# Performance work log

Measured on AMD Instinct MI355X. Metric: run time of the kernel, lower is better.

The kernel has to match this reference:

```python
import jax, jax.numpy as jnp
import numpy as np

H = 12          # num_heads
E = 768         # key_dim
LORA_SCALE = 32.0 / 4.0  # scale / R
NEG = -1e9


def setup_inputs() -> dict:
    key = jax.random.key(0)
    ks = jax.random.split(key, 8)
    B, L = 2, 2048
    return {
        "x": jax.random.normal(ks[0], (B, L, E), jnp.float32),
        "w_in": jax.random.normal(ks[1], (E, 3 * E), jnp.float32) * 0.02,
        "b_in": jnp.zeros((3 * E,), jnp.float32),
        "A_in": jax.random.normal(ks[2], (4, 3 * E), jnp.float32) * 0.02,
        "B_in": jax.random.normal(ks[3], (E, 4), jnp.float32) * 0.02,
        "w_out": jax.random.normal(ks[4], (E, E), jnp.float32) * 0.02,
        "b_out": jnp.zeros((E,), jnp.float32),
        "A_out": jax.random.normal(ks[5], (4, E), jnp.float32) * 0.02,
        "B_out": jax.random.normal(ks[6], (E, 4), jnp.float32) * 0.02,
    }


def reference(x, w_in, b_in, A_in, B_in, w_out, b_out, A_out, B_out):
    Bb, L, _ = x.shape
    D = E // H
    # LoRA-adapted input projection: w + (scale/R) * B @ A
    w1 = w_in + LORA_SCALE * (B_in @ A_in)          # [E, 3E]
    c = jnp.einsum('ble,eo->blo', x, w1) + b_in      # [B, L, 3E]
    q, k, v = jnp.split(c, 3, axis=2)
    # split heads -> [B, H, L, D]
    def heads(t):
        return t.reshape(Bb, L, H, D).transpose(0, 2, 1, 3)
    q, k, v = heads(q), heads(k), heads(v)
    # attention scores (no 1/sqrt(d): scale=False in module defaults)
    w = jnp.einsum('bhqd,bhkd->bhqk', q, k)          # [B, H, L, L]
    band = jnp.tril(jnp.ones((L, L), jnp.float32))   # causal band
    w = w * band + NEG * (1.0 - band)
    w = jax.nn.softmax(w, axis=-1)
    a = jnp.einsum('bhqk,bhkd->bhqd', w, v)          # [B, H, L, D]
    a = a.transpose(0, 2, 1, 3).reshape(Bb, L, E)    # merge heads
    w2 = w_out + LORA_SCALE * (B_out @ A_out)        # [E, E]
    return jnp.einsum('ble,eo->blo', a, w2) + b_out
```

## Files before the change

### kernel.cpp

```cpp
#include <hip/hip_runtime.h>
#include <hip/hip_bf16.h>

#define BB 2
#define LL 2048
#define EE 768
#define HH 12
#define DD 64
#define N3 2304
#define TOK 4096
#define LOG2E 1.4426950408889634f

typedef __attribute__((ext_vector_type(8))) short short8;
typedef __attribute__((ext_vector_type(4))) short s16x4;
typedef __attribute__((ext_vector_type(4))) float f32x4;
typedef __attribute__((ext_vector_type(4))) unsigned int uix4;
typedef unsigned int uint_t;
typedef unsigned short ushort_t;

__device__ __forceinline__ f32x4 mfma16(short8 a, short8 b, f32x4 c) {
  return __builtin_amdgcn_mfma_f32_16x16x32_bf16(a, b, c, 0, 0, 0);
}
__device__ __forceinline__ f32x4 mfma16k16(s16x4 a, s16x4 b, f32x4 c) {
  return __builtin_amdgcn_mfma_f32_16x16x16bf16_1k(a, b, c, 0, 0, 0);
}

__device__ __forceinline__ ushort_t bf16bits(float f) {
  __hip_bfloat16 h = __float2bfloat16(f);
  return *reinterpret_cast<ushort_t*>(&h);
}

__device__ __forceinline__ uint_t pack2bf(float a, float b) {
  return (uint_t)bf16bits(a) | ((uint_t)bf16bits(b) << 16);
}

__device__ __forceinline__ float bits2f(ushort_t u) {
  union { uint_t u; float f; } cv;
  cv.u = ((uint_t)u) << 16;
  return cv.f;
}

__device__ __forceinline__ void stage64(const __hip_bfloat16* gbase, int ldg,
                                        short* lds, int tid) {
  const int wave = tid >> 6, lane = tid & 63;
#pragma unroll
  for (int c = 0; c < 4; ++c) {
    int off = c * 4096 + wave * 1024 + lane * 16;
    int row = off >> 7;
    int cs  = (off & 127) >> 4;
    int cc  = cs ^ (row & 7);
    __builtin_amdgcn_global_load_lds(
        (const __attribute__((address_space(1))) void*)((const short*)gbase + (size_t)row * ldg + cc * 8),
        (__attribute__((address_space(3))) void*)(lds + c * 2048 + wave * 512),
        16, 0, 0);
  }
}

__device__ __forceinline__ void stage128(const __hip_bfloat16* gbase, int ldg,
                                         short* lds, int tid) {
  const int wave = tid >> 6, lane = tid & 63;
#pragma unroll
  for (int c = 0; c < 4; ++c) {
    int off = c * 4096 + wave * 1024 + lane * 16;
    int row = off >> 8;
    int cs  = (off & 255) >> 4;
    int cc  = cs ^ (row & 7);
    __builtin_amdgcn_global_load_lds(
        (const __attribute__((address_space(1))) void*)((const short*)gbase + (size_t)row * ldg + cc * 8),
        (__attribute__((address_space(3))) void*)(lds + c * 2048 + wave * 512),
        16, 0, 0);
  }
}

__device__ __forceinline__ short8 frag64(const short* lds, int row, int chunk) {
  return *(const short8*)(lds + row * 64 + (chunk ^ (row & 7)) * 8);
}

__global__ void prep_kernel(const float* __restrict__ x, const float* __restrict__ w_in,
                            const float* __restrict__ A_in, const float* __restrict__ B_in,
                            const float* __restrict__ w_out, const float* __restrict__ A_out,
                            const float* __restrict__ B_out,
                            __hip_bfloat16* __restrict__ xb, __hip_bfloat16* __restrict__ w1T,
                            __hip_bfloat16* __restrict__ w2T) {
  __shared__ float tile[32][33];
  const int bid = blockIdx.x, t = threadIdx.x;
  if (bid < 2304) {
    const float *W, *Am, *Bm;
    __hip_bfloat16* out;
    int N, tx, ty;
    if (bid < 1728) { W = w_in;  Am = A_in;  Bm = B_in;  out = w1T; N = N3; tx = bid % 72; ty = bid / 72; }
    else { int jj = bid - 1728; W = w_out; Am = A_out; Bm = B_out; out = w2T; N = EE; tx = jj % 24; ty = jj / 24; }
    const int e0 = ty * 32, o0 = tx * 32;
    const int r = t >> 5, col = t & 31;
#pragma unroll
    for (int i = 0; i < 4; ++i)
      tile[r + i * 8][col] = W[(size_t)(e0 + r + i * 8) * N + (o0 + col)];
    __syncthreads();
    const int e = e0 + col;
    const float b0 = Bm[e * 4 + 0], b1 = Bm[e * 4 + 1], b2 = Bm[e * 4 + 2], b3 = Bm[e * 4 + 3];
#pragma unroll
    for (int i = 0; i < 4; ++i) {
      const int o = o0 + r + i * 8;
      float acc = b0 * Am[o] + b1 * Am[N + o] + b2 * Am[2 * N + o] + b3 * Am[3 * N + o];
      out[(size_t)o * EE + e] = __float2bfloat16(tile[col][r + i * 8] + 8.0f * acc);
    }
  } else {
    const int j = bid - 2304;
    const float* src = x + (size_t)j * 4096 + t * 16;
    short* dst = (short*)xb + (size_t)j * 4096 + t * 16;
#pragma unroll
    for (int half = 0; half < 2; ++half) {
      float4 a = ((const float4*)src)[half * 2];
      float4 b = ((const float4*)src)[half * 2 + 1];
      short8 v;
      v[0] = (short)bf16bits(a.x); v[1] = (short)bf16bits(a.y);
      v[2] = (short)bf16bits(a.z); v[3] = (short)bf16bits(a.w);
      v[4] = (short)bf16bits(b.x); v[5] = (short)bf16bits(b.y);
      v[6] = (short)bf16bits(b.z); v[7] = (short)bf16bits(b.w);
      ((short8*)dst)[half] = v;
    }
  }
}

template<bool F32OUT, bool QSCALE, bool SPLITV>
__global__ __launch_bounds__(256, 2) void gemm_bt(const __hip_bfloat16* __restrict__ A,
                                                  const __hip_bfloat16* __restrict__ BT,
                                                  const float* __restrict__ bias,
                                                  void* __restrict__ outp,
                                                  __hip_bfloat16* __restrict__ vTp,
                                                  int M, int N, int K) {
  __shared__ __align__(16) short Al[128 * 64];
  __shared__ __align__(16) short Bl[128 * 64];
  const int tid = threadIdx.x, lane = tid & 63, wave = tid >> 6;
  const int quad = lane >> 4, c16 = lane & 15;
  const int n0 = blockIdx.x * 128, m0 = blockIdx.y * 128;
  const int msub = (wave & 1) * 64, nsub = (wave >> 1) * 64;
  f32x4 acc[4][4] = {};
  for (int k0 = 0; k0 < K; k0 += 64) {
    __syncthreads();
    stage64(A + (size_t)m0 * K + k0, K, Al, tid);
    stage64(BT + (size_t)n0 * K + k0, K, Bl, tid);
    __syncthreads();
#pragma unroll
    for (int ks = 0; ks < 2; ++ks) {
      short8 af[4], bfr[4];
#pragma unroll
      for (int i = 0; i < 4; ++i) {
        af[i]  = frag64(Al, msub + i * 16 + c16, ks * 4 + quad);
        bfr[i] = frag64(Bl, nsub + i * 16 + c16, ks * 4 + quad);
      }
#pragma unroll
      for (int mi = 0; mi < 4; ++mi)
#pragma unroll
        for (int ni = 0; ni < 4; ++ni)
          acc[mi][ni] = mfma16(af[mi], bfr[ni], acc[mi][ni]);
    }
  }
  if (SPLITV && n0 >= 2 * EE) {
    const int bofs = (m0 >> 11) * EE;
    const int l0 = (m0 & 2047) + msub;
#pragma unroll
    for (int ni = 0; ni < 4; ++ni) {
      int n = n0 + nsub + ni * 16 + c16;
      float bv = bias[n];
      const size_t rowbase = (size_t)(bofs + (n - 2 * EE)) * LL;
#pragma unroll
      for (int mi = 0; mi < 4; ++mi) {
        int l = l0 + mi * 16 + quad * 4;
        uint2 w;
        w.x = pack2bf(acc[mi][ni][0] + bv, acc[mi][ni][1] + bv);
        w.y = pack2bf(acc[mi][ni][2] + bv, acc[mi][ni][3] + bv);
        *(uint2*)((short*)vTp + rowbase + l) = w;
      }
    }
    return;
  }
#pragma unroll
  for (int ni = 0; ni < 4; ++ni) {
    int n = n0 + nsub + ni * 16 + c16;
    float bv = bias[n];
    float sc = (QSCALE && n < EE) ? LOG2E : 1.0f;
#pragma unroll
    for (int mi = 0; mi < 4; ++mi) {
      int row0 = m0 + msub + mi * 16 + quad * 4;
#pragma unroll
      for (int r = 0; r < 4; ++r) {
        float v = (acc[mi][ni][r] + bv) * sc;
        if (F32OUT) ((float*)outp)[(size_t)(row0 + r) * N + n] = v;
        else ((__hip_bfloat16*)outp)[(size_t)(row0 + r) * N + n] = __float2bfloat16(v);
      }
    }
  }
}

#define SLOT_BYTES 16896
union pk4 { uint_t u[2]; s16x4 s4; };

__global__ __launch_bounds__(256, 2) void attn_kernel(const __hip_bfloat16* __restrict__ qkv,
                                                      const __hip_bfloat16* __restrict__ vT,
                                                      char* __restrict__ Opart,
                                                      __hip_bfloat16* __restrict__ abuf) {
  __shared__ __align__(16) short Kl[2 * 128 * 64];
  __shared__ __align__(16) short Vl[2 * 64 * 128];
  const int tid = threadIdx.x, lane = tid & 63, wave = tid >> 6;
  const int quad = lane >> 4, c16 = lane & 15;
  const int bid = blockIdx.x;
  const int bh = bid % 24;
  const int j = bid / 24;
  int qt, cch;
  if (j < 8)       { qt = 8 + j;  cch = 0; }
  else if (j < 16) { qt = 23 - j; cch = 1; }
  else             { qt = 23 - j; cch = 0; }
  const int b = bh / HH, h = bh % HH;
  const int q0 = qt * 128;
  const int qw = q0 + wave * 32;
  const int ks = cch * 1024;
  const int ke = min(q0 + 128, ks + 1024);
  const int niter = (ke - ks + 127) >> 7;
  short8 qfA[2], qfB[2];
  {
    const short* qra = (const short*)qkv + (size_t)(b * LL + qw + c16) * N3 + h * DD;
    qfA[0] = *(const short8*)(qra + quad * 8);
    qfA[1] = *(const short8*)(qra + 32 + quad * 8);
    const short* qrb = qra + 16 * N3;
    qfB[0] = *(const short8*)(qrb + quad * 8);
    qfB[1] = *(const short8*)(qrb + 32 + quad * 8);
  }
  float lA = 0.f, lB = 0.f;
  f32x4 oA[4] = {}, oB[4] = {};
  const int vsub = (quad & 1) * 4;
  const int cxor = (c16 & 7);
  const __hip_bfloat16* kgbase = qkv + (size_t)(b * LL) * N3 + EE + h * DD;
  const __hip_bfloat16* vgbase = vT + (size_t)((b * HH + h) * DD) * LL;
  stage64(kgbase + (size_t)ks * N3, N3, Kl, tid);
  stage128(vgbase + ks, LL, Vl, tid);
  for (int it = 0; it < niter; ++it) {
    const int k0 = ks + it * 128;
    __syncthreads();
    if (it + 1 < niter) {
      short* Kn = Kl + ((it + 1) & 1) * 8192;
      short* Vn = Vl + ((it + 1) & 1) * 8192;
      stage64(kgbase + (size_t)(k0 + 128) * N3, N3, Kn, tid);
      stage128(vgbase + k0 + 128, LL, Vn, tid);
    }
    const short* Kb = Kl + (it & 1) * 8192;
    const short* Vb = Vl + (it & 1) * 8192;
    int nlimB = (qw + 31 - k0) / 16 + 1; if (nlimB > 8) nlimB = 8;
    int nlimA = (qw + 15 - k0) / 16 + 1; if (nlimA > 8) nlimA = 8;
#pragma unroll
    for (int nt = 0; nt < 8; ++nt) {
      if (nt < nlimB) {
        const short* krow = Kb + (nt * 16 + c16) * 64;
        const int kc0 = (quad ^ cxor) * 8;
        short8 kf0 = *(const short8*)(krow + kc0);
        short8 kf1 = *(const short8*)(krow + (kc0 ^ 32));
        const int kb = k0 + nt * 16 + quad * 4;
        const bool diag = (k0 + nt * 16 + 15 > qw + 16);
        f32x4 sB = {};
        sB = mfma16(kf0, qfB[0], sB);
        sB = mfma16(kf1, qfB[1], sB);
        if (diag) {
          const int q = qw + 16 + c16;
#pragma unroll
          for (int r = 0; r < 4; ++r)
            if (kb + r > q) sB[r] = -1e9f;
        }
        pk4 pB;
        {
          float p0 = exp2f(sB[0]), p1 = exp2f(sB[1]);
          float p2 = exp2f(sB[2]), p3 = exp2f(sB[3]);
          lB += (p0 + p1) + (p2 + p3);
          pB.u[0] = pack2bf(p0, p1);
          pB.u[1] = pack2bf(p2, p3);
        }
        const bool doA = (nt < nlimA);
        pk4 pA;
        if (doA) {
          f32x4 sA = {};
          sA = mfma16(kf0, qfA[0], sA);
          sA = mfma16(kf1, qfA[1], sA);
          if (k0 + nt * 16 + 15 > qw) {
            const int q = qw + c16;
#pragma unroll
            for (int r = 0; r < 4; ++r)
              if (kb + r > q) sA[r] = -1e9f;
          }
          float p0 = exp2f(sA[0]), p1 = exp2f(sA[1]);
          float p2 = exp2f(sA[2]), p3 = exp2f(sA[3]);
          lA += (p0 + p1) + (p2 + p3);
          pA.u[0] = pack2bf(p0, p1);
          pA.u[1] = pack2bf(p2, p3);
        }
        const int cg = nt * 2 + (quad >> 1);
        const short* vbase = Vb + c16 * 128 + ((cg ^ cxor) * 8 + vsub);
#pragma unroll
        for (int dt = 0; dt < 4; ++dt) {
          s16x4 vf = *(const s16x4*)(vbase + dt * 2048);
          oB[dt] = mfma16k16(vf, pB.s4, oB[dt]);
          if (doA) oA[dt] = mfma16k16(vf, pA.s4, oA[dt]);
        }
      }
    }
  }
  lA += __shfl_xor(lA, 16); lA += __shfl_xor(lA, 32);
  lB += __shfl_xor(lB, 16); lB += __shfl_xor(lB, 32);
  const bool single = (cch == 0) && (qt < 8);
  const float nA = single ? 1.0f / lA : 1.0f;
  const float nB = single ? 1.0f / lB : 1.0f;
  char* op = Opart + (size_t)((bh * 16 + qt) * 2 + cch) * SLOT_BYTES;
  __syncthreads();
  if (!single && quad == 0) {
    float* lout = (float*)(op + 16384);
    lout[wave * 32 + c16] = lA;
    lout[wave * 32 + 16 + c16] = lB;
  }
  short* reg = Kl + wave * 1152;
#pragma unroll
  for (int hh = 0; hh < 2; ++hh) {
    const float sc = hh ? nB : nA;
#pragma unroll
    for (int dt = 0; dt < 4; ++dt) {
      f32x4 o = hh ? oB[dt] : oA[dt];
      uint_t* p = (uint_t*)(reg + c16 * 72 + dt * 16 + quad * 4);
      p[0] = pack2bf(o[0] * sc, o[1] * sc);
      p[1] = pack2bf(o[2] * sc, o[3] * sc);
    }
#pragma unroll
    for (int it = 0; it < 2; ++it) {
      int idx = it * 64 + lane;
      int tq = idx >> 3, c = idx & 7;
      short8 v = *(const short8*)(reg + tq * 72 + c * 8);
      if (single)
        *(short8*)((short*)abuf + (size_t)(b * LL + q0 + wave * 32 + hh * 16 + tq) * EE + h * DD + c * 8) = v;
      else
        *(short8*)((short*)op + (wave * 32 + hh * 16 + tq) * 64 + c * 8) = v;
    }
  }
}

__global__ void merge_kernel(const char* __restrict__ Opart,
                             __hip_bfloat16* __restrict__ abuf) {
  const int t = threadIdx.x;
  const int bh = blockIdx.x >> 3, qt = 8 + (blockIdx.x & 7);
  const int b = bh / HH, h = bh % HH;
  const char* p0 = Opart + (size_t)((bh * 16 + qt) * 2) * SLOT_BYTES;
  const char* p1 = p0 + SLOT_BYTES;
  const int q = t >> 1, dc = (t & 1) * 32;
  float l = ((const float*)(p0 + 16384))[q] + ((const float*)(p1 + 16384))[q];
  const float inv = 1.0f / l;
  const short* o0 = (const short*)p0 + q * 64 + dc;
  const short* o1 = (const short*)p1 + q * 64 + dc;
  __align__(16) short out[32];
#pragma unroll
  for (int blk = 0; blk < 4; ++blk) {
    short8 r0 = *(const short8*)(o0 + blk * 8);
    short8 r1 = *(const short8*)(o1 + blk * 8);
#pragma unroll
    for (int i = 0; i < 8; ++i) {
      float v = bits2f((ushort_t)r0[i]) + bits2f((ushort_t)r1[i]);
      out[blk * 8 + i] = (short)bf16bits(v * inv);
    }
  }
  short* dst = (short*)abuf + (size_t)(b * LL + qt * 128 + q) * EE + h * DD + dc;
#pragma unroll
  for (int blk = 0; blk < 4; ++blk)
    *(short8*)(dst + blk * 8) = *(short8*)(out + blk * 8);
}

extern "C" void kernel_launch(void* const* d_in, const int* in_sizes, int n_in,
                              void* d_out, int out_size, void* d_ws, size_t ws_size,
                              hipStream_t stream) {
  (void)in_sizes; (void)n_in; (void)out_size; (void)ws_size;
  const float* x     = (const float*)d_in[0];
  const float* w_in  = (const float*)d_in[1];
  const float* b_in  = (const float*)d_in[2];
  const float* A_in  = (const float*)d_in[3];
  const float* B_in  = (const float*)d_in[4];
  const float* w_out = (const float*)d_in[5];
  const float* b_out = (const float*)d_in[6];
  const float* A_out = (const float*)d_in[7];
  const float* B_out = (const float*)d_in[8];
  char* ws = (char*)d_ws;
  __hip_bfloat16* xb   = (__hip_bfloat16*)(ws);
  __hip_bfloat16* w1T  = (__hip_bfloat16*)(ws + 6291456);
  __hip_bfloat16* w2T  = (__hip_bfloat16*)(ws + 9830400);
  __hip_bfloat16* qkv  = (__hip_bfloat16*)(ws + 11010048);
  __hip_bfloat16* vT   = (__hip_bfloat16*)(ws + 29884416);
  __hip_bfloat16* abuf = (__hip_bfloat16*)(ws + 36175872);
  char* Opart          = ws + 42467328;

  prep_kernel<<<3072, 256, 0, stream>>>(x, w_in, A_in, B_in, w_out, A_out, B_out,
                                        xb, w1T, w2T);
  gemm_bt<false, true, true><<<dim3(N3 / 128, TOK / 128), 256, 0, stream>>>(
      xb, w1T, b_in, qkv, vT, TOK, N3, EE);
  attn_kernel<<<24 * 24, 256, 0, stream>>>(qkv, vT, Opart, abuf);
  merge_kernel<<<24 * 8, 256, 0, stream>>>(Opart, abuf);
  gemm_bt<true, false, false><<<dim3(EE / 128, TOK / 128), 256, 0, stream>>>(
      abuf, w2T, b_out, d_out, nullptr, TOK, EE, EE);
}
```

Before: 169.6 us.

## Split attention KV into 512-chunks, read K/V directly from global, fast exp2

Attention now splits the key range into up to four 512-token chunks instead of two 1024-token chunks, launching 40 work items per head through lookup tables, with the merge kernel summing up to four partials. The LDS double-buffered staging of K and V is removed: fragments are loaded straight from global memory, which frees shared memory so occupancy can rise (launch bounds 4). exp2f is replaced by the raw v_exp_f32 instruction, and bf16 packing uses a simple bias-add rounding. The aim is better load balance and occupancy, at the cost of uncoalesced, cache-dependent global fragment loads, extra partial-merge traffic, and slightly different rounding (no NaN handling).

Result: slower. 207.3 us (+22.2%).

```diff
diff --git a/kernel.cpp b/kernel.cpp
--- a/kernel.cpp
+++ b/kernel.cpp
@@ -29,8 +29,16 @@
   return *reinterpret_cast<ushort_t*>(&h);
 }
 
-__device__ __forceinline__ uint_t pack2bf(float a, float b) {
-  return (uint_t)bf16bits(a) | ((uint_t)bf16bits(b) << 16);
+__device__ __forceinline__ float fast_exp2(float x) {
+  float r;
+  asm("v_exp_f32 %0, %1" : "=v"(r) : "v"(x));
+  return r;
+}
+
+__device__ __forceinline__ uint_t pack2bf_rn(float a, float b) {
+  uint_t ua = __float_as_uint(a) + 0x8000u;
+  uint_t ub = __float_as_uint(b) + 0x8000u;
+  return (ua >> 16) | (ub & 0xFFFF0000u);
 }
 
 __device__ __forceinline__ float bits2f(ushort_t u) {
@@ -47,22 +55,6 @@
     int off = c * 4096 + wave * 1024 + lane * 16;
     int row = off >> 7;
     int cs  = (off & 127) >> 4;
-    int cc  = cs ^ (row & 7);
-    __builtin_amdgcn_global_load_lds(
-        (const __attribute__((address_space(1))) void*)((const short*)gbase + (size_t)row * ldg + cc * 8),
-        (__attribute__((address_space(3))) void*)(lds + c * 2048 + wave * 512),
-        16, 0, 0);
-  }
-}
-
-__device__ __forceinline__ void stage128(const __hip_bfloat16* gbase, int ldg,
-                                         short* lds, int tid) {
-  const int wave = tid >> 6, lane = tid & 63;
-#pragma unroll
-  for (int c = 0; c < 4; ++c) {
-    int off = c * 4096 + wave * 1024 + lane * 16;
-    int row = off >> 8;
-    int cs  = (off & 255) >> 4;
     int cc  = cs ^ (row & 7);
     __builtin_amdgcn_global_load_lds(
         (const __attribute__((address_space(1))) void*)((const short*)gbase + (size_t)row * ldg + cc * 8),
@@ -167,8 +159,8 @@
       for (int mi = 0; mi < 4; ++mi) {
         int l = l0 + mi * 16 + quad * 4;
         uint2 w;
-        w.x = pack2bf(acc[mi][ni][0] + bv, acc[mi][ni][1] + bv);
-        w.y = pack2bf(acc[mi][ni][2] + bv, acc[mi][ni][3] + bv);
+        w.x = pack2bf_rn(acc[mi][ni][0] + bv, acc[mi][ni][1] + bv);
+        w.y = pack2bf_rn(acc[mi][ni][2] + bv, acc[mi][ni][3] + bv);
         *(uint2*)((short*)vTp + rowbase + l) = w;
       }
     }
@@ -195,26 +187,29 @@
 #define SLOT_BYTES 16896
 union pk4 { uint_t u[2]; s16x4 s4; };
 
-__global__ __launch_bounds__(256, 2) void attn_kernel(const __hip_bfloat16* __restrict__ qkv,
+__device__ const signed char QTAB[40] = {
+  3,4,5,6,7,8,9,10,11,12,13,14,15,  7,8,9,10,11,12,13,14,15,
+  11,12,13,14,15, 15,  2,6,10,14,  1,5,9,13,  0,4,8,12};
+__device__ const signed char CTAB[40] = {
+  0,0,0,0,0,0,0,0,0,0,0,0,0,  1,1,1,1,1,1,1,1,1,
+  2,2,2,2,2, 3,  0,1,2,3,  0,1,2,3,  0,1,2,3};
+
+__global__ __launch_bounds__(256, 4) void attn_kernel(const __hip_bfloat16* __restrict__ qkv,
                                                       const __hip_bfloat16* __restrict__ vT,
                                                       char* __restrict__ Opart,
                                                       __hip_bfloat16* __restrict__ abuf) {
-  __shared__ __align__(16) short Kl[2 * 128 * 64];
-  __shared__ __align__(16) short Vl[2 * 64 * 128];
+  __shared__ __align__(16) short Ep[4 * 1152];
   const int tid = threadIdx.x, lane = tid & 63, wave = tid >> 6;
   const int quad = lane >> 4, c16 = lane & 15;
   const int bid = blockIdx.x;
   const int bh = bid % 24;
   const int j = bid / 24;
-  int qt, cch;
-  if (j < 8)       { qt = 8 + j;  cch = 0; }
-  else if (j < 16) { qt = 23 - j; cch = 1; }
-  else             { qt = 23 - j; cch = 0; }
+  const int qt = QTAB[j], cch = CTAB[j];
   const int b = bh / HH, h = bh % HH;
   const int q0 = qt * 128;
   const int qw = q0 + wave * 32;
-  const int ks = cch * 1024;
-  const int ke = min(q0 + 128, ks + 1024);
+  const int ks = cch * 512;
+  const int ke = min(q0 + 128, ks + 512);
   const int niter = (ke - ks + 127) >> 7;
   short8 qfA[2], qfB[2];
   {
@@ -227,32 +222,18 @@
   }
   float lA = 0.f, lB = 0.f;
   f32x4 oA[4] = {}, oB[4] = {};
-  const int vsub = (quad & 1) * 4;
-  const int cxor = (c16 & 7);
-  const __hip_bfloat16* kgbase = qkv + (size_t)(b * LL) * N3 + EE + h * DD;
-  const __hip_bfloat16* vgbase = vT + (size_t)((b * HH + h) * DD) * LL;
-  stage64(kgbase + (size_t)ks * N3, N3, Kl, tid);
-  stage128(vgbase + ks, LL, Vl, tid);
+  const short* kg = (const short*)qkv + (size_t)(b * LL + c16) * N3 + EE + h * DD + quad * 8;
+  const short* vg = (const short*)vT + (size_t)((b * HH + h) * DD + c16) * LL + quad * 4;
   for (int it = 0; it < niter; ++it) {
     const int k0 = ks + it * 128;
-    __syncthreads();
-    if (it + 1 < niter) {
-      short* Kn = Kl + ((it + 1) & 1) * 8192;
-      short* Vn = Vl + ((it + 1) & 1) * 8192;
-      stage64(kgbase + (size_t)(k0 + 128) * N3, N3, Kn, tid);
-      stage128(vgbase + k0 + 128, LL, Vn, tid);
-    }
-    const short* Kb = Kl + (it & 1) * 8192;
-    const short* Vb = Vl + (it & 1) * 8192;
     int nlimB = (qw + 31 - k0) / 16 + 1; if (nlimB > 8) nlimB = 8;
     int nlimA = (qw + 15 - k0) / 16 + 1; if (nlimA > 8) nlimA = 8;
 #pragma unroll
     for (int nt = 0; nt < 8; ++nt) {
       if (nt < nlimB) {
-        const short* krow = Kb + (nt * 16 + c16) * 64;
-        const int kc0 = (quad ^ cxor) * 8;
-        short8 kf0 = *(const short8*)(krow + kc0);
-        short8 kf1 = *(const short8*)(krow + (kc0 ^ 32));
+        const short* kr = kg + (size_t)(k0 + nt * 16) * N3;
+        short8 kf0 = *(const short8*)(kr);
+        short8 kf1 = *(const short8*)(kr + 32);
         const int kb = k0 + nt * 16 + quad * 4;
         const bool diag = (k0 + nt * 16 + 15 > qw + 16);
         f32x4 sB = {};
@@ -266,11 +247,11 @@
         }
         pk4 pB;
         {
-          float p0 = exp2f(sB[0]), p1 = exp2f(sB[1]);
-          float p2 = exp2f(sB[2]), p3 = exp2f(sB[3]);
+          float p0 = fast_exp2(sB[0]), p1 = fast_exp2(sB[1]);
+          float p2 = fast_exp2(sB[2]), p3 = fast_exp2(sB[3]);
           lB += (p0 + p1) + (p2 + p3);
-          pB.u[0] = pack2bf(p0, p1);
-          pB.u[1] = pack2bf(p2, p3);
+          pB.u[0] = pack2bf_rn(p0, p1);
+          pB.u[1] = pack2bf_rn(p2, p3);
         }
         const bool doA = (nt < nlimA);
         pk4 pA;
@@ -284,17 +265,16 @@
             for (int r = 0; r < 4; ++r)
               if (kb + r > q) sA[r] = -1e9f;
           }
-          float p0 = exp2f(sA[0]), p1 = exp2f(sA[1]);
-          float p2 = exp2f(sA[2]), p3 = exp2f(sA[3]);
+          float p0 = fast_exp2(sA[0]), p1 = fast_exp2(sA[1]);
+          float p2 = fast_exp2(sA[2]), p3 = fast_exp2(sA[3]);
           lA += (p0 + p1) + (p2 + p3);
-          pA.u[0] = pack2bf(p0, p1);
-          pA.u[1] = pack2bf(p2, p3);
+          pA.u[0] = pack2bf_rn(p0, p1);
+          pA.u[1] = pack2bf_rn(p2, p3);
         }
-        const int cg = nt * 2 + (quad >> 1);
-        const short* vbase = Vb + c16 * 128 + ((cg ^ cxor) * 8 + vsub);
+        const short* vb = vg + k0 + nt * 16;
 #pragma unroll
         for (int dt = 0; dt < 4; ++dt) {
-          s16x4 vf = *(const s16x4*)(vbase + dt * 2048);
+          s16x4 vf = *(const s16x4*)(vb + (size_t)dt * 16 * LL);
           oB[dt] = mfma16k16(vf, pB.s4, oB[dt]);
           if (doA) oA[dt] = mfma16k16(vf, pA.s4, oA[dt]);
         }
@@ -303,17 +283,16 @@
   }
   lA += __shfl_xor(lA, 16); lA += __shfl_xor(lA, 32);
   lB += __shfl_xor(lB, 16); lB += __shfl_xor(lB, 32);
-  const bool single = (cch == 0) && (qt < 8);
+  const bool single = (cch == 0) && (qt < 4);
   const float nA = single ? 1.0f / lA : 1.0f;
   const float nB = single ? 1.0f / lB : 1.0f;
-  char* op = Opart + (size_t)((bh * 16 + qt) * 2 + cch) * SLOT_BYTES;
-  __syncthreads();
+  char* op = Opart + (size_t)((bh * 16 + qt) * 4 + cch) * SLOT_BYTES;
   if (!single && quad == 0) {
     float* lout = (float*)(op + 16384);
     lout[wave * 32 + c16] = lA;
     lout[wave * 32 + 16 + c16] = lB;
   }
-  short* reg = Kl + wave * 1152;
+  short* reg = Ep + wave * 1152;
 #pragma unroll
   for (int hh = 0; hh < 2; ++hh) {
     const float sc = hh ? nB : nA;
@@ -321,8 +300,8 @@
     for (int dt = 0; dt < 4; ++dt) {
       f32x4 o = hh ? oB[dt] : oA[dt];
       uint_t* p = (uint_t*)(reg + c16 * 72 + dt * 16 + quad * 4);
-      p[0] = pack2bf(o[0] * sc, o[1] * sc);
-      p[1] = pack2bf(o[2] * sc, o[3] * sc);
+      p[0] = pack2bf_rn(o[0] * sc, o[1] * sc);
+      p[1] = pack2bf_rn(o[2] * sc, o[3] * sc);
     }
 #pragma unroll
     for (int it = 0; it < 2; ++it) {
@@ -340,26 +319,34 @@
 __global__ void merge_kernel(const char* __restrict__ Opart,
                              __hip_bfloat16* __restrict__ abuf) {
   const int t = threadIdx.x;
-  const int bh = blockIdx.x >> 3, qt = 8 + (blockIdx.x & 7);
+  const int bh = blockIdx.x / 12, qt = 4 + (blockIdx.x % 12);
+  const int nch = (qt >> 2) + 1;
   const int b = bh / HH, h = bh % HH;
-  const char* p0 = Opart + (size_t)((bh * 16 + qt) * 2) * SLOT_BYTES;
-  const char* p1 = p0 + SLOT_BYTES;
+  const char* pb = Opart + (size_t)((bh * 16 + qt) * 4) * SLOT_BYTES;
   const int q = t >> 1, dc = (t & 1) * 32;
-  float l = ((const float*)(p0 + 16384))[q] + ((const float*)(p1 + 16384))[q];
+  float l = 0.f;
+  float acc[32];
+#pragma unroll
+  for (int i = 0; i < 32; ++i) acc[i] = 0.f;
+#pragma unroll
+  for (int c = 0; c < 4; ++c) {
+    if (c < nch) {
+      const char* p = pb + (size_t)c * SLOT_BYTES;
+      l += ((const float*)(p + 16384))[q];
+      const short* o = (const short*)p + q * 64 + dc;
+#pragma unroll
+      for (int blk = 0; blk < 4; ++blk) {
+        short8 r = *(const short8*)(o + blk * 8);
+#pragma unroll
+        for (int i = 0; i < 8; ++i) acc[blk * 8 + i] += bits2f((ushort_t)r[i]);
+      }
+    }
+  }
   const float inv = 1.0f / l;
-  const short* o0 = (const short*)p0 + q * 64 + dc;
-  const short* o1 = (const short*)p1 + q * 64 + dc;
   __align__(16) short out[32];
 #pragma unroll
-  for (int blk = 0; blk < 4; ++blk) {
-    short8 r0 = *(const short8*)(o0 + blk * 8);
-    short8 r1 = *(const short8*)(o1 + blk * 8);
-#pragma unroll
-    for (int i = 0; i < 8; ++i) {
-      float v = bits2f((ushort_t)r0[i]) + bits2f((ushort_t)r1[i]);
-      out[blk * 8 + i] = (short)bf16bits(v * inv);
-    }
-  }
+  for (int i = 0; i < 16; ++i)
+    ((uint_t*)out)[i] = pack2bf_rn(acc[2 * i] * inv, acc[2 * i + 1] * inv);
   short* dst = (short*)abuf + (size_t)(b * LL + qt * 128 + q) * EE + h * DD + dc;
 #pragma unroll
   for (int blk = 0; blk < 4; ++blk)
@@ -392,8 +379,8 @@
                                         xb, w1T, w2T);
   gemm_bt<false, true, true><<<dim3(N3 / 128, TOK / 128), 256, 0, stream>>>(
       xb, w1T, b_in, qkv, vT, TOK, N3, EE);
-  attn_kernel<<<24 * 24, 256, 0, stream>>>(qkv, vT, Opart, abuf);
-  merge_kernel<<<24 * 8, 256, 0, stream>>>(Opart, abuf);
+  attn_kernel<<<24 * 40, 256, 0, stream>>>(qkv, vT, Opart, abuf);
+  merge_kernel<<<24 * 12, 256, 0, stream>>>(Opart, abuf);
   gemm_bt<true, false, false><<<dim3(EE / 128, TOK / 128), 256, 0, stream>>>(
       abuf, w2T, b_out, d_out, nullptr, TOK, EE, EE);
 }
```
